# Performance work log

Measured on AMD Instinct MI355X. Metric: run time of the kernel, lower is better.

Reference implementation:

```python
import jax, jax.numpy as jnp
import numpy as np

B, L, D = 8, 2048, 1024
NH, M = 32, 16            # TTTConfig defaults: num_attention_heads=32, mini_batch_size=16
HD = D // NH              # 32
NM = L // M               # 128 mini-batches
DI = 2048                 # FFN hidden (configs.d_lower)
BASE_LR = 1.0
EPS = 1e-6


def setup_inputs() -> dict:
    key = jax.random.key(0)
    ks = jax.random.split(key, 12)
    n = lambda k, s, sc=0.02: jax.random.normal(k, s, jnp.float32) * sc
    return dict(
        enc_input=jax.random.normal(ks[0], (B, L, D), jnp.float32),
        ln0_g=jnp.ones((D,), jnp.float32), ln0_b=jnp.zeros((D,), jnp.float32),
        Wq=n(ks[1], (D, D)), Wk=n(ks[2], (D, D)), Wv=n(ks[3], (D, D)), Wo=n(ks[4], (D, D)),
        W1=n(ks[5], (NH, HD, HD)), b1=jnp.zeros((NH, 1, HD), jnp.float32),
        token_idx_delta=jnp.zeros((M,), jnp.float32),
        lr_w=n(ks[6], (NH, D)), lr_b=jnp.zeros((NH,), jnp.float32),
        ttt_ln_g=jnp.ones((NH, HD), jnp.float32), ttt_ln_b=jnp.zeros((NH, HD), jnp.float32),
        post_g=jnp.ones((D,), jnp.float32), post_b=jnp.zeros((D,), jnp.float32),
        ffn_g=jnp.ones((D,), jnp.float32), ffn_b=jnp.zeros((D,), jnp.float32),
        fw1=n(ks[7], (D, DI)), fb1=jnp.zeros((DI,), jnp.float32),
        fw2=n(ks[8], (DI, D)), fb2=jnp.zeros((D,), jnp.float32),
    )


def _layernorm(x, g, b):
    mu = x.mean(-1, keepdims=True)
    v = ((x - mu) ** 2).mean(-1, keepdims=True)
    return (x - mu) * jax.lax.rsqrt(v + EPS) * g + b


def _rope(x):
    # x: [B,NH,L,HD]; standard rotary embedding, theta=10000
    half = HD // 2
    inv = 1.0 / (10000.0 ** (jnp.arange(0, HD, 2, dtype=jnp.float32) / HD))
    pos = jnp.arange(L, dtype=jnp.float32)
    fr = pos[:, None] * inv[None, :]                    # [L, HD/2]
    emb = jnp.concatenate([fr, fr], -1)                 # [L, HD]
    cos, sin = jnp.cos(emb), jnp.sin(emb)
    rot = jnp.concatenate([-x[..., half:], x[..., :half]], -1)
    return x * cos + rot * sin


def reference(enc_input, ln0_g, ln0_b, Wq, Wk, Wv, Wo, W1, b1, token_idx_delta,
              lr_w, lr_b, ttt_ln_g, ttt_ln_b, post_g, post_b,
              ffn_g, ffn_b, fw1, fb1, fw2, fb2):
    residual = enc_input
    x = _layernorm(enc_input, ln0_g, ln0_b)

    def heads(t):  # [B,L,D] -> [B,NH,L,HD]
        return t.reshape(B, L, NH, HD).transpose(0, 2, 1, 3)

    XQ = _rope(heads(x @ Wq))
    XK = _rope(heads(x @ Wk))
    XV = heads(x @ Wv)

    # per-token learnable learning rates (sigmoid gate), token_idx schedule
    X_mb = x.reshape(B, NM, M, D)
    ttt_lr = jax.nn.sigmoid(jnp.einsum('bnkc,hc->bhnk', X_mb, lr_w) + lr_b[None, :, None, None])
    ttt_lr_eta = BASE_LR * ttt_lr / HD                               # [B,NH,NM,M]
    token_idx = jnp.clip(1.0 / jnp.arange(1, M + 1, dtype=jnp.float32) + token_idx_delta, 0.0, None)
    eta = token_idx[None, None, None, :, None] * ttt_lr_eta[:, :, :, None, :]  # [B,NH,NM,M,M]

    def to_scan(t):  # [B,NH,L,HD] -> [NM,B,NH,M,HD]
        return t.reshape(B, NH, NM, M, HD).transpose(2, 0, 1, 3, 4)

    xs = (to_scan(XQ), to_scan(XK), to_scan(XV), eta.transpose(2, 0, 1, 3, 4))

    lw = ttt_ln_g[:, None, :]   # [NH,1,HD]
    lb = ttt_ln_b[:, None, :]
    tril = jnp.tril(jnp.ones((M, M), jnp.float32))

    def ln_fwd(z):
        mu = z.mean(-1, keepdims=True)
        v = ((z - mu) ** 2).mean(-1, keepdims=True)
        return (z - mu) * jax.lax.rsqrt(v + EPS) * lw + lb

    def ln_l2_bwd(z, tgt):
        # gradient of 0.5*||LN(z)-tgt||^2 w.r.t. z (fused LN l2 backward)
        mu = z.mean(-1, keepdims=True)
        v = ((z - mu) ** 2).mean(-1, keepdims=True)
        std = jnp.sqrt(v + EPS)
        xhat = (z - mu) / std
        gxh = (xhat * lw + lb - tgt) * lw
        return (HD * gxh - gxh.sum(-1, keepdims=True)
                - xhat * (gxh * xhat).sum(-1, keepdims=True)) / (HD * std)

    W1_0 = jnp.broadcast_to(W1[None], (B, NH, HD, HD))
    b1_0 = jnp.broadcast_to(b1[None], (B, NH, 1, HD))

    def step(carry, inp):
        W, bvec = carry
        q, k, v_, e = inp                                    # [B,NH,M,HD], e: [B,NH,M,M]
        Z1 = k @ W + bvec
        grad = ln_l2_bwd(Z1, v_ - k)                         # [B,NH,M,HD]
        Attn1 = tril * (q @ k.transpose(0, 1, 3, 2))         # causal dual-form attention
        b_bar = bvec - (tril * e) @ grad
        Z1_bar = q @ W - (e * Attn1) @ grad + b_bar
        last_e = e[:, :, -1, :, None]                        # [B,NH,M,1]
        W_new = W - (last_e * k).transpose(0, 1, 3, 2) @ grad
        b_new = bvec - (last_e * grad).sum(-2, keepdims=True)
        return (W_new, b_new), q + ln_fwd(Z1_bar)

    _, outs = jax.lax.scan(step, (W1_0, b1_0), xs)           # [NM,B,NH,M,HD]
    out = outs.transpose(1, 0, 3, 2, 4).reshape(B, L, D)     # -> [B,L,D]
    out = _layernorm(out, post_g, post_b) @ Wo               # post_norm + o_proj
    out = out + residual                                     # dropout = identity (eval)

    # PositionWiseFeedForward (pre-LN, residual)
    r2 = out
    h = _layernorm(out, ffn_g, ffn_b)
    h = jax.nn.relu(h @ fw1 + fb1) @ fw2 + fb2
    return h + r2
```

## Files before the change

### kernel.cpp

```cpp
#include <hip/hip_runtime.h>
#include <hip/hip_bf16.h>
#include <stdint.h>

#define B_   8
#define L_   2048
#define D_   1024
#define NH_  32
#define M_   16
#define NM_  128
#define HD_  32
#define DI_  2048
#define BL_  16384
#define EPS_ 1e-6f

typedef __attribute__((ext_vector_type(8))) short  s16x8;
typedef __attribute__((ext_vector_type(4))) short  s16x4;
typedef __attribute__((ext_vector_type(8))) __bf16 bf16x8;
typedef __attribute__((ext_vector_type(4))) float  f32x4;
typedef __attribute__((ext_vector_type(4))) unsigned u32x4;

__device__ __forceinline__ float bf2f(short s){
  unsigned u = ((unsigned)(unsigned short)s) << 16;
  return __builtin_bit_cast(float, u);
}
__device__ __forceinline__ short f2bf(float f){
  unsigned u = __builtin_bit_cast(unsigned, f);
  u = u + 0x7FFFu + ((u >> 16) & 1u);
  return (short)(u >> 16);
}
__device__ __forceinline__ unsigned cvtpk(float lo, float hi){
  unsigned r;
  asm("v_cvt_pk_bf16_f32 %0, %1, %2" : "=v"(r) : "v"(lo), "v"(hi));
  return r;
}
template<int N>
__device__ __forceinline__ float ror_add(float v){
  const int y = __builtin_amdgcn_update_dpp(
      0, __builtin_bit_cast(int, v), 0x120 + N, 0xF, 0xF, true);
  return v + __builtin_bit_cast(float, y);
}
__device__ __forceinline__ float rsum16d(float v){
  v = ror_add<1>(v); v = ror_add<2>(v); v = ror_add<4>(v); v = ror_add<8>(v);
  return v;
}
__device__ __forceinline__ void wgbar(){
  asm volatile("s_waitcnt lgkmcnt(0)" ::: "memory");
  __builtin_amdgcn_s_barrier();
  __builtin_amdgcn_sched_barrier(0);
}
__device__ __forceinline__ void gl16(const void* g, void* l){
  __builtin_amdgcn_global_load_lds(
      (const __attribute__((address_space(1))) void*)g,
      (__attribute__((address_space(3))) void*)l, 16, 0, 0);
}

__global__ __launch_bounds__(256) void transpose_cast(
    const float* __restrict__ in, short* __restrict__ out, int R, int Cc)
{
  __shared__ float t[32][33];
  const int lx = threadIdx.x & 31, ly = threadIdx.x >> 5;
  const int r0 = blockIdx.y * 32, c0 = blockIdx.x * 32;
  #pragma unroll
  for (int s = 0; s < 4; ++s){
    const int r = ly + s*8;
    t[r][lx] = in[(size_t)(r0 + r)*Cc + c0 + lx];
  }
  __syncthreads();
  #pragma unroll
  for (int s = 0; s < 4; ++s){
    const int r = ly + s*8;
    out[(size_t)(c0 + r)*R + r0 + lx] = f2bf(t[lx][r]);
  }
}

struct TC4 { const float *s0,*s1,*s2,*s3; short *d0,*d1,*d2,*d3; };
__global__ __launch_bounds__(256) void transpose_cast4(TC4 p)
{
  __shared__ float t[32][33];
  const int z = blockIdx.z;
  const float* in = (z==0)?p.s0:(z==1)?p.s1:(z==2)?p.s2:p.s3;
  short* out      = (z==0)?p.d0:(z==1)?p.d1:(z==2)?p.d2:p.d3;
  const int lx = threadIdx.x & 31, ly = threadIdx.x >> 5;
  const int r0 = blockIdx.y * 32, c0 = blockIdx.x * 32;
  #pragma unroll
  for (int s = 0; s < 4; ++s){
    const int r = ly + s*8;
    t[r][lx] = in[(size_t)(r0 + r)*1024 + c0 + lx];
  }
  __syncthreads();
  #pragma unroll
  for (int s = 0; s < 4; ++s){
    const int r = ly + s*8;
    out[(size_t)(c0 + r)*1024 + r0 + lx] = f2bf(t[lx][r]);
  }
}

__global__ __launch_bounds__(256) void misc_prep(
    const float* __restrict__ lr_w, short* __restrict__ lrwb,
    float* __restrict__ ct, float* __restrict__ st)
{
  const int idx = blockIdx.x*256 + threadIdx.x;
  if (idx < NH_*D_){
    lrwb[idx] = f2bf(lr_w[idx]);
  } else {
    const int k = idx - NH_*D_;
    const int l = k >> 4, j = k & 15;
    const float inv = powf(10000.f, -(float)j * (1.f/16.f));
    const float fr  = (float)l * inv;
    ct[k] = cosf(fr);
    st[k] = sinf(fr);
  }
}

__global__ __launch_bounds__(256) void ln_rows(
    const float* __restrict__ in, const float* __restrict__ g,
    const float* __restrict__ bta, short* __restrict__ out)
{
  const int row = blockIdx.x, tid = threadIdx.x;
  const float4 v = ((const float4*)(in + (size_t)row*D_))[tid];
  float s  = v.x + v.y + v.z + v.w;
  float s2 = v.x*v.x + v.y*v.y + v.z*v.z + v.w*v.w;
  #pragma unroll
  for (int m = 1; m < 64; m <<= 1){ s += __shfl_xor(s, m); s2 += __shfl_xor(s2, m); }
  __shared__ float rs[4], rq[4];
  if ((tid & 63) == 0){ rs[tid>>6] = s; rq[tid>>6] = s2; }
  __syncthreads();
  s  = rs[0] + rs[1] + rs[2] + rs[3];
  s2 = rq[0] + rq[1] + rq[2] + rq[3];
  const float mu   = s  * (1.f/D_);
  const float var  = s2 * (1.f/D_) - mu*mu;
  const float rstd = rsqrtf(var + EPS_);
  const float4 gg = ((const float4*)g)[tid];
  const float4 bb = ((const float4*)bta)[tid];
  s16x4 o;
  o[0] = f2bf((v.x - mu)*rstd*gg.x + bb.x);
  o[1] = f2bf((v.y - mu)*rstd*gg.y + bb.y);
  o[2] = f2bf((v.z - mu)*rstd*gg.z + bb.z);
  o[3] = f2bf((v.w - mu)*rstd*gg.w + bb.w);
  ((s16x4*)(out + (size_t)row*D_))[tid] = o;
}

__global__ __launch_bounds__(256) void ln_rows_bf(
    const short* __restrict__ in, const float* __restrict__ g,
    const float* __restrict__ bta, short* __restrict__ out)
{
  const int row = blockIdx.x, tid = threadIdx.x;
  const s16x4 v4 = ((const s16x4*)(in + (size_t)row*D_))[tid];
  float v[4];
  #pragma unroll
  for (int e = 0; e < 4; ++e) v[e] = bf2f(v4[e]);
  float s  = v[0]+v[1]+v[2]+v[3];
  float s2 = v[0]*v[0]+v[1]*v[1]+v[2]*v[2]+v[3]*v[3];
  #pragma unroll
  for (int m = 1; m < 64; m <<= 1){ s += __shfl_xor(s, m); s2 += __shfl_xor(s2, m); }
  __shared__ float rs[4], rq[4];
  if ((tid & 63) == 0){ rs[tid>>6] = s; rq[tid>>6] = s2; }
  __syncthreads();
  s  = rs[0] + rs[1] + rs[2] + rs[3];
  s2 = rq[0] + rq[1] + rq[2] + rq[3];
  const float mu   = s  * (1.f/D_);
  const float var  = s2 * (1.f/D_) - mu*mu;
  const float rstd = rsqrtf(var + EPS_);
  const float4 gg = ((const float4*)g)[tid];
  const float4 bb = ((const float4*)bta)[tid];
  s16x4 o;
  #pragma unroll
  for (int e = 0; e < 4; ++e){
    const float gv = (e==0)?gg.x:(e==1)?gg.y:(e==2)?gg.z:gg.w;
    const float bv = (e==0)?bb.x:(e==1)?bb.y:(e==2)?bb.z:bb.w;
    o[e] = f2bf((v[e] - mu)*rstd*gv + bv);
  }
  ((s16x4*)(out + (size_t)row*D_))[tid] = o;
}

template<int ACT, int OUTBF, int BIAS, int RES, int RESB, int QKVOUT>
__global__ __launch_bounds__(512, 2) void gemm256(
    const short* __restrict__ A, const short* __restrict__ Bt,
    const float* __restrict__ bias, const float* __restrict__ res,
    const short* __restrict__ resb,
    float* __restrict__ Cf, short* __restrict__ Cb,
    const float* __restrict__ ct, const float* __restrict__ st,
    int Mr, int N, int K)
{
  __shared__ __align__(16) short As[4][8192];
  __shared__ __align__(16) short Bs[4][8192];
  const int tid  = threadIdx.x;
  const int lane = tid & 63, wid = tid >> 6;
  const int wr = wid >> 2, wc = wid & 3;
  const int nwg = gridDim.x * gridDim.y;
  const int wg  = blockIdx.y * gridDim.x + blockIdx.x;
  const int swz = (wg & 7) * (nwg >> 3) + (wg >> 3);
  const int bx  = swz % gridDim.x, by = swz / gridDim.x;
  const int row0 = by * 256, col0 = bx * 256;

  f32x4 acc[8][4] = {};

  const int kswz = (((tid & 3) ^ ((tid >> 3) & 3)) << 3);
  const short* gAb = A  + (size_t)(row0 + (tid >> 2)) * K + kswz;
  const short* gBb = Bt + (size_t)(col0 + (tid >> 2)) * K + kswz;
  short* lAb = &As[0][0] + tid*8;
  short* lBb = &Bs[0][0] + tid*8;

  auto stage = [&](int bt2, int t2){
    const size_t kb = (size_t)t2 * 32;
    gl16(gAb + kb,                   lAb + bt2*8192);
    gl16(gAb + kb + 128*(size_t)K,   lAb + bt2*8192 + 4096);
    gl16(gBb + kb,                   lBb + bt2*8192);
    gl16(gBb + kb + 128*(size_t)K,   lBb + bt2*8192 + 4096);
  };

  const int fr = lane & 15;
  const int k0 = (((lane >> 4) ^ ((lane >> 1) & 3)) << 3);

  const int nK = K >> 5;
  stage(0, 0); stage(1, 1); stage(2, 2);
  asm volatile("s_waitcnt vmcnt(8)" ::: "memory");
  __builtin_amdgcn_s_barrier();

  for (int kt = 0; kt < nK; ++kt){
    const int bt = kt & 3;
    const short* Ab = &As[0][0] + bt*8192 + wr*4096;
    const short* Bb = &Bs[0][0] + bt*8192 + (wc >> 1)*4096 + (wc & 1)*2048;
    bf16x8 af[8], bfv[4];
    #pragma unroll
    for (int m = 0; m < 8; ++m)
      af[m] = *(const bf16x8*)(Ab + (m*16 + fr)*32 + k0);
    #pragma unroll
    for (int n = 0; n < 4; ++n)
      bfv[n] = *(const bf16x8*)(Bb + (n*16 + fr)*32 + k0);
    if (kt + 3 < nK) stage((kt + 3) & 3, kt + 3);
    __builtin_amdgcn_s_setprio(1);
    #pragma unroll
    for (int m = 0; m < 8; ++m)
      #pragma unroll
      for (int n = 0; n < 4; ++n)
        acc[m][n] = __builtin_amdgcn_mfma_f32_16x16x32_bf16(af[m], bfv[n], acc[m][n], 0,0,0);
    __builtin_amdgcn_s_setprio(0);
    if (kt + 3 < nK)      asm volatile("s_waitcnt vmcnt(8)" ::: "memory");
    else if (kt + 2 < nK) asm volatile("s_waitcnt vmcnt(4)" ::: "memory");
    else if (kt + 1 < nK) asm volatile("s_waitcnt vmcnt(0)" ::: "memory");
    __builtin_amdgcn_s_barrier();
  }

  const int cr = (lane >> 4) * 4, cc = lane & 15;
  if (QKVOUT){
    const int part = col0 >> 10;
    #pragma unroll
    for (int m = 0; m < 8; ++m){
      const int gr0 = row0 + wr*128 + m*16 + cr;
      const int bidx = gr0 >> 11, l0 = gr0 & (L_-1);
      const int nn = l0 >> 4;
      if (part < 2){
        #pragma unroll
        for (int np = 0; np < 2; ++np){
          const int gc = col0 + wc*64 + np*32 + cc;
          const int hh = (gc & 1023) >> 5;
          short* tile = Cb + ((size_t)(bidx*NH_ + hh)*NM_ + nn)*2048;
          s16x4 r0v, r1v;
          #pragma unroll
          for (int r = 0; r < 4; ++r){
            const int l = l0 + r;
            const float cv = ct[l*16 + cc], sv = st[l*16 + cc];
            const float x0 = acc[m][np*2][r], x1 = acc[m][np*2+1][r];
            const short q0 = f2bf(x0*cv - x1*sv);
            const short q1 = f2bf(x1*cv + x0*sv);
            tile[part*512 + (cr + r)*32 + cc]      = q0;
            tile[part*512 + (cr + r)*32 + cc + 16] = q1;
            r0v[r] = q0; r1v[r] = q1;
          }
          if (part == 1){
            *(s16x4*)(tile + 1024 + cc*16 + cr)      = r0v;
            *(s16x4*)(tile + 1024 + (cc+16)*16 + cr) = r1v;
          }
        }
      } else {
        #pragma unroll
        for (int n = 0; n < 4; ++n){
          const int gc = col0 + wc*64 + n*16 + cc;
          const int hh = (gc & 1023) >> 5, dd = gc & 31;
          short* tile = Cb + ((size_t)(bidx*NH_ + hh)*NM_ + nn)*2048;
          s16x4 p;
          #pragma unroll
          for (int r = 0; r < 4; ++r) p[r] = f2bf(acc[m][n][r]);
          *(s16x4*)(tile + 1536 + dd*16 + cr) = p;
        }
      }
    }
    return;
  }
  #pragma unroll
  for (int m = 0; m < 8; ++m){
    #pragma unroll
    for (int n = 0; n < 4; ++n){
      const int gc = col0 + wc*64 + n*16 + cc;
      float bv = 0.f;
      if (BIAS) bv = bias[gc];
      #pragma unroll
      for (int r = 0; r < 4; ++r){
        const int gr = row0 + wr*128 + m*16 + cr + r;
        float v = acc[m][n][r] + bv;
        if (RES)  v += res[(size_t)gr*N + gc];
        if (RESB) v += bf2f(resb[(size_t)gr*N + gc]);
        if (ACT == 1) v = fmaxf(v, 0.f);
        if (OUTBF) Cb[(size_t)gr*N + gc] = f2bf(v);
        else       Cf[(size_t)gr*N + gc] = v;
      }
    }
  }
}

__global__ __launch_bounds__(256) void eta_kernel(
    const short* __restrict__ xb, const short* __restrict__ lrwb,
    const float* __restrict__ lr_b, float* __restrict__ eta)
{
  __shared__ __align__(16) short wl[NH_*1032];
  const int tid = threadIdx.x;
  const int lane = tid & 63, wv = tid >> 6;
  const int li = lane & 15, lh = lane >> 4;
  #pragma unroll
  for (int s = 0; s < 16; ++s){
    const int e = tid + 256*s;
    const int hrow = e >> 7, c = (e & 127) * 8;
    *(s16x8*)(wl + hrow*1032 + c) = ((const s16x8*)lrwb)[e];
  }
  __syncthreads();

  const int t0 = (blockIdx.x*4 + wv) * 16;
  const short* xrow = xb + (size_t)(t0 + li)*1024 + 8*lh;
  const short* w0p = wl + li*1032 + 8*lh;
  const short* w1p = wl + (16 + li)*1032 + 8*lh;
  f32x4 acc0 = {}, acc1 = {};
  #pragma unroll 4
  for (int s = 0; s < 32; ++s){
    const bf16x8 a  = *(const bf16x8*)(xrow + s*32);
    const bf16x8 b0 = *(const bf16x8*)(w0p + s*32);
    const bf16x8 b1 = *(const bf16x8*)(w1p + s*32);
    acc0 = __builtin_amdgcn_mfma_f32_16x16x32_bf16(a, b0, acc0, 0,0,0);
    acc1 = __builtin_amdgcn_mfma_f32_16x16x32_bf16(a, b1, acc1, 0,0,0);
  }
  const int t = t0 + 4*lh;
  const int bidx = t >> 11, l = t & (L_-1), n = l >> 4, im = l & 15;
  float* e0 = eta + ((size_t)(bidx*NH_ + li)*NM_ + n)*M_ + im;
  float* e1 = eta + ((size_t)(bidx*NH_ + 16 + li)*NM_ + n)*M_ + im;
  const float lb0 = lr_b[li], lb1 = lr_b[16 + li];
  #pragma unroll
  for (int r = 0; r < 4; ++r){
    e0[r] = 1.f/(1.f + __expf(-(acc0[r] + lb0))) * (1.f/32.f);
    e1[r] = 1.f/(1.f + __expf(-(acc1[r] + lb1))) * (1.f/32.f);
  }
}

__global__ __launch_bounds__(128) void scan_kernel(
    const short* __restrict__ Q5, const float* __restrict__ eta,
    const float* __restrict__ W1, const float* __restrict__ b1,
    const float* __restrict__ tdelta, const float* __restrict__ lng,
    const float* __restrict__ lnb, short* __restrict__ out)
{
  const int bh = blockIdx.x;
  const int h = bh & 31, b = bh >> 5;
  const int lane = threadIdx.x & 63;
  const int wv = threadIdx.x >> 6;
  const int li = lane & 15, lh = lane >> 4;

  __shared__ __align__(16) short WTl[2][32*40];
  __shared__ __align__(16) short GTl[2][32*24];
  __shared__ float BBl[2][2][16];
  __shared__ __align__(16) float AT[16*20];
  __shared__ __align__(16) short QLl[2][16*40];

  const short* chain = Q5 + (size_t)bh * (NM_*2048);
  const float* ech   = eta + (size_t)bh * (NM_*16);

  float lw[2], lbv[2];
  #pragma unroll
  for (int hh = 0; hh < 2; ++hh){
    lw[hh]  = lng[h*32 + 16*hh + li];
    lbv[hh] = lnb[h*32 + 16*hh + li];
  }

  if (wv == 0){
    f32x4 Wq[2][2];
    #pragma unroll
    for (int rb = 0; rb < 2; ++rb)
      #pragma unroll
      for (int cb = 0; cb < 2; ++cb)
        #pragma unroll
        for (int r = 0; r < 4; ++r)
          Wq[rb][cb][r] = W1[h*1024 + (16*rb + 4*lh + r)*32 + 16*cb + li];
    float bb[2];
    bb[0] = b1[h*32 + li];  bb[1] = b1[h*32 + 16 + li];
    const float lef = fmaxf(1.f/16.f + tdelta[15], 0.f);

    auto writeWT = [&](int sl){
      #pragma unroll
      for (int cb = 0; cb < 2; ++cb)
        #pragma unroll
        for (int rb = 0; rb < 2; ++rb){
          const unsigned p0 = cvtpk(Wq[rb][cb][0], Wq[rb][cb][1]);
          const unsigned p1 = cvtpk(Wq[rb][cb][2], Wq[rb][cb][3]);
          *(uint64_t*)(&WTl[sl][0] + (16*cb + li)*40 + 16*rb + 4*lh) =
              ((uint64_t)p1 << 32) | p0;
        }
    };
    auto readWf = [&](int sl, bf16x8* Wf){
      Wf[0] = *(const bf16x8*)(&WTl[sl][0] + li*40 + 8*lh);
      Wf[1] = *(const bf16x8*)(&WTl[sl][0] + (16 + li)*40 + 8*lh);
    };

    writeWT(0);
    if (lh == 0){ BBl[0][0][li] = bb[0]; BBl[0][1][li] = bb[1]; }
    bf16x8 Wf[2];
    readWf(0, Wf);

    struct P0 { s16x8 kA, kTq0, kTq1; s16x4 kTe0, kTe1, vTe0, vTe1;
                f32x4 lr0, lr1, lr2, lr3; };
    auto ld0 = [&](int n) -> P0 {
      const short* t = chain + (size_t)n*2048;
      const float* e = ech + n*16;
      P0 p;
      p.kA   = *(const s16x8*)(t + 512 + li*32 + 8*lh);
      p.kTq0 = *(const s16x8*)(t + 1024 + li*16 + 8*(lh & 1));
      p.kTq1 = *(const s16x8*)(t + 1024 + (16 + li)*16 + 8*(lh & 1));
      p.kTe0 = *(const s16x4*)(t + 1024 + li*16 + 4*lh);
      p.kTe1 = *(const s16x4*)(t + 1024 + (16 + li)*16 + 4*lh);
      p.vTe0 = *(const s16x4*)(t + 1536 + li*16 + 4*lh);
      p.vTe1 = *(const s16x4*)(t + 1536 + (16 + li)*16 + 4*lh);
      p.lr0 = *(const f32x4*)(e);     p.lr1 = *(const f32x4*)(e + 4);
      p.lr2 = *(const f32x4*)(e + 8); p.lr3 = *(const f32x4*)(e + 12);
      return p;
    };

    P0 cur = ld0(0);
    wgbar();

    const int gcol = (8*lh) & 15;
    #pragma unroll 1
    for (int n = 0; n < NM_; ++n){
      const int sl = n & 1;
      P0 nxt = ld0(n + 1 < NM_ ? n + 1 : NM_ - 1);
      const bf16x8 kAf = __builtin_bit_cast(bf16x8, cur.kA);

      f32x4 zac[2];
      #pragma unroll
      for (int hh = 0; hh < 2; ++hh){
        f32x4 c0; c0[0]=bb[hh]; c0[1]=bb[hh]; c0[2]=bb[hh]; c0[3]=bb[hh];
        zac[hh] = __builtin_amdgcn_mfma_f32_16x16x32_bf16(kAf, Wf[hh], c0, 0,0,0);
      }

      float xh[2][4], grad[2][4], rstdv[4];
      #pragma unroll
      for (int r = 0; r < 4; ++r){
        float s  = rsum16d(zac[0][r] + zac[1][r]);
        float q2 = rsum16d(zac[0][r]*zac[0][r] + zac[1][r]*zac[1][r]);
        const float mu  = s * (1.f/32.f);
        const float var = q2 * (1.f/32.f) - mu*mu;
        const float rstd = rsqrtf(var + EPS_);
        rstdv[r] = rstd;
        xh[0][r] = (zac[0][r] - mu) * rstd;
        xh[1][r] = (zac[1][r] - mu) * rstd;
      }
      #pragma unroll
      for (int r = 0; r < 4; ++r){
        const float t0 = bf2f(cur.vTe0[r]) - bf2f(cur.kTe0[r]);
        const float t1 = bf2f(cur.vTe1[r]) - bf2f(cur.kTe1[r]);
        const float g0 = (xh[0][r]*lw[0] + lbv[0] - t0)*lw[0];
        const float g1 = (xh[1][r]*lw[1] + lbv[1] - t1)*lw[1];
        const float sg  = rsum16d(g0 + g1);
        const float sgx = rsum16d(g0*xh[0][r] + g1*xh[1][r]);
        const float f = rstdv[r] * (1.f/32.f);
        grad[0][r] = (32.f*g0 - sg - xh[0][r]*sgx) * f;
        grad[1][r] = (32.f*g1 - sg - xh[1][r]*sgx) * f;
      }

      #pragma unroll
      for (int hh = 0; hh < 2; ++hh){
        const unsigned p0 = cvtpk(grad[hh][0], grad[hh][1]);
        const unsigned p1 = cvtpk(grad[hh][2], grad[hh][3]);
        *(uint64_t*)(&GTl[sl][0] + (16*hh + li)*24 + 4*lh) =
            ((uint64_t)p1 << 32) | p0;
      }
      bf16x8 gf[2];
      gf[0] = *(const bf16x8*)(&GTl[sl][0] + li*24 + gcol);
      gf[1] = *(const bf16x8*)(&GTl[sl][0] + (16 + li)*24 + gcol);

      const f32x4 plA = (lh & 1) ? cur.lr2 : cur.lr0;
      const f32x4 plB = (lh & 1) ? cur.lr3 : cur.lr1;
      #pragma unroll
      for (int rb = 0; rb < 2; ++rb){
        const s16x8 kq = rb ? cur.kTq1 : cur.kTq0;
        float av8[8];
        #pragma unroll
        for (int jj = 0; jj < 8; ++jj){
          const float lrv = (jj < 4) ? plA[jj] : plB[jj - 4];
          av8[jj] = (lh < 2) ? -lef * lrv * bf2f(kq[jj]) : 0.f;
        }
        u32x4 auv;
        auv[0] = cvtpk(av8[0], av8[1]); auv[1] = cvtpk(av8[2], av8[3]);
        auv[2] = cvtpk(av8[4], av8[5]); auv[3] = cvtpk(av8[6], av8[7]);
        const bf16x8 af = __builtin_bit_cast(bf16x8, auv);
        #pragma unroll
        for (int cb = 0; cb < 2; ++cb)
          Wq[rb][cb] = __builtin_amdgcn_mfma_f32_16x16x32_bf16(af, gf[cb], Wq[rb][cb], 0,0,0);
      }

      writeWT(sl ^ 1);
      readWf(sl ^ 1, Wf);

      f32x4 lrq;
      { const f32x4 t0 = (lh & 1) ? cur.lr1 : cur.lr0;
        const f32x4 t1 = (lh & 1) ? cur.lr3 : cur.lr2;
        lrq = (lh & 2) ? t1 : t0; }
      #pragma unroll
      for (int hh = 0; hh < 2; ++hh){
        float t = 0.f;
        #pragma unroll
        for (int r = 0; r < 4; ++r) t += lrq[r]*grad[hh][r];
        t += __shfl_xor(t, 16); t += __shfl_xor(t, 32);
        bb[hh] -= lef * t;
      }
      if (lh == 0){ BBl[sl ^ 1][0][li] = bb[0]; BBl[sl ^ 1][1][li] = bb[1]; }
      cur = nxt;
      wgbar();
    }
  } else {
    const float tok_i = fmaxf(1.f/(float)(li+1) + tdelta[li], 0.f);
    short* outp = out + (size_t)b*L_*D_ + h*32;
    const int gcol = (8*lh) & 15;

    struct P1 { s16x8 qA, kA; f32x4 lr0, lr1, lr2, lr3; };
    auto ld1 = [&](int n) -> P1 {
      const short* t = chain + (size_t)n*2048;
      const float* e = ech + n*16;
      P1 p;
      p.qA = *(const s16x8*)(t + li*32 + 8*lh);
      p.kA = *(const s16x8*)(t + 512 + li*32 + 8*lh);
      p.lr0 = *(const f32x4*)(e);     p.lr1 = *(const f32x4*)(e + 4);
      p.lr2 = *(const f32x4*)(e + 8); p.lr3 = *(const f32x4*)(e + 12);
      return p;
    };

    auto outln = [&](int n, const f32x4* yac){
      #pragma unroll
      for (int r = 0; r < 4; ++r){
        const float s  = rsum16d(yac[0][r] + yac[1][r]);
        const float q2 = rsum16d(yac[0][r]*yac[0][r] + yac[1][r]*yac[1][r]);
        const float mu   = s * (1.f/32.f);
        const float var  = q2 * (1.f/32.f) - mu*mu;
        const float rstd = rsqrtf(var + EPS_);
        const int row = 4*lh + r;
        #pragma unroll
        for (int hh = 0; hh < 2; ++hh){
          const float qv = bf2f(QLl[n & 1][row*40 + 16*hh + li]);
          const float o  = qv + (yac[hh][r] - mu)*rstd*lw[hh] + lbv[hh];
          outp[(size_t)(n*16 + row)*D_ + 16*hh + li] = f2bf(o);
        }
      }
    };

    P1 cur = ld1(0);
    wgbar();

    f32x4 yprev[2] = {};
    bf16x8 pPrev = {};
    #pragma unroll 1
    for (int n = 0; n < NM_; ++n){
      const int sl = n & 1;
      bf16x8 Wf0 = *(const bf16x8*)(&WTl[sl][0] + li*40 + 8*lh);
      bf16x8 Wf1 = *(const bf16x8*)(&WTl[sl][0] + (16 + li)*40 + 8*lh);
      const float bb0 = BBl[sl][0][li];
      const float bb1 = BBl[sl][1][li];

      if (n > 0){
        bf16x8 gf0 = *(const bf16x8*)(&GTl[sl ^ 1][0] + li*24 + gcol);
        bf16x8 gf1 = *(const bf16x8*)(&GTl[sl ^ 1][0] + (16 + li)*24 + gcol);
        yprev[0] = __builtin_amdgcn_mfma_f32_16x16x32_bf16(pPrev, gf0, yprev[0], 0,0,0);
        yprev[1] = __builtin_amdgcn_mfma_f32_16x16x32_bf16(pPrev, gf1, yprev[1], 0,0,0);
        outln(n - 1, yprev);
      }

      P1 nxt = ld1(n + 1 < NM_ ? n + 1 : NM_ - 1);
      const bf16x8 qAf = __builtin_bit_cast(bf16x8, cur.qA);
      const bf16x8 kAf = __builtin_bit_cast(bf16x8, cur.kA);

      *(s16x8*)(&QLl[sl][0] + li*40 + 8*lh) = cur.qA;

      f32x4 aac = {};
      aac = __builtin_amdgcn_mfma_f32_16x16x32_bf16(qAf, kAf, aac, 0,0,0);
      #pragma unroll
      for (int r = 0; r < 4; ++r)
        AT[(4*lh + r)*20 + li] = aac[r];

      f32x4 arA = {}, arB = {};
      if (lh < 2){
        arA = *(const f32x4*)(AT + li*20 + 8*lh);
        arB = *(const f32x4*)(AT + li*20 + 8*lh + 4);
      }
      const f32x4 plA = (lh & 1) ? cur.lr2 : cur.lr0;
      const f32x4 plB = (lh & 1) ? cur.lr3 : cur.lr1;
      float pv[8];
      #pragma unroll
      for (int jj = 0; jj < 8; ++jj){
        const float av  = (jj < 4) ? arA[jj] : arB[jj - 4];
        const float lrv = (jj < 4) ? plA[jj] : plB[jj - 4];
        const bool ok = (lh < 2) && (8*lh + jj <= li);
        pv[jj] = ok ? -tok_i * lrv * (1.f + av) : 0.f;
      }
      u32x4 ppv;
      ppv[0] = cvtpk(pv[0], pv[1]); ppv[1] = cvtpk(pv[2], pv[3]);
      ppv[2] = cvtpk(pv[4], pv[5]); ppv[3] = cvtpk(pv[6], pv[7]);
      pPrev = __builtin_bit_cast(bf16x8, ppv);

      { f32x4 c0; c0[0]=bb0; c0[1]=bb0; c0[2]=bb0; c0[3]=bb0;
        yprev[0] = __builtin_amdgcn_mfma_f32_16x16x32_bf16(qAf, Wf0, c0, 0,0,0); }
      { f32x4 c0; c0[0]=bb1; c0[1]=bb1; c0[2]=bb1; c0[3]=bb1;
        yprev[1] = __builtin_amdgcn_mfma_f32_16x16x32_bf16(qAf, Wf1, c0, 0,0,0); }

      cur = nxt;
      wgbar();
    }
    {
      const int sl = (NM_ - 1) & 1;
      bf16x8 gf0 = *(const bf16x8*)(&GTl[sl][0] + li*24 + gcol);
      bf16x8 gf1 = *(const bf16x8*)(&GTl[sl][0] + (16 + li)*24 + gcol);
      yprev[0] = __builtin_amdgcn_mfma_f32_16x16x32_bf16(pPrev, gf0, yprev[0], 0,0,0);
      yprev[1] = __builtin_amdgcn_mfma_f32_16x16x32_bf16(pPrev, gf1, yprev[1], 0,0,0);
      outln(NM_ - 1, yprev);
    }
  }
}

extern "C" void kernel_launch(void* const* d_in, const int* in_sizes, int n_in,
                              void* d_out, int out_size, void* d_ws, size_t ws_size,
                              hipStream_t stream)
{
  const float* enc    = (const float*)d_in[0];
  const float* ln0_g  = (const float*)d_in[1];
  const float* ln0_b  = (const float*)d_in[2];
  const float* Wq     = (const float*)d_in[3];
  const float* Wk     = (const float*)d_in[4];
  const float* Wv     = (const float*)d_in[5];
  const float* Wo     = (const float*)d_in[6];
  const float* W1     = (const float*)d_in[7];
  const float* b1     = (const float*)d_in[8];
  const float* tdelta = (const float*)d_in[9];
  const float* lr_w   = (const float*)d_in[10];
  const float* lr_b   = (const float*)d_in[11];
  const float* ttt_g  = (const float*)d_in[12];
  const float* ttt_b  = (const float*)d_in[13];
  const float* post_g = (const float*)d_in[14];
  const float* post_b = (const float*)d_in[15];
  const float* ffn_g  = (const float*)d_in[16];
  const float* ffn_b  = (const float*)d_in[17];
  const float* fw1    = (const float*)d_in[18];
  const float* fb1    = (const float*)d_in[19];
  const float* fw2    = (const float*)d_in[20];
  const float* fb2    = (const float*)d_in[21];

  char* ws = (char*)d_ws;
  short* Q5    = (short*)(ws + 0);
  short* XB    = (short*)(ws + 134217728);
  short* SCANB = (short*)(ws + 134217728);
  short* WQKVT = (short*)(ws + 167772160);
  short* WOT   = (short*)(ws + 174063616);
  short* FW1T  = (short*)(ws + 176160768);
  short* FW2T  = (short*)(ws + 180355072);
  short* LRWB  = (short*)(ws + 184549376);
  float* CT    = (float*)(ws + 184614912);
  float* ST    = (float*)(ws + 184745984);
  float* ETA   = (float*)(ws + 184877056);
  short* YB    = (short*)(ws + 0);
  short* HB    = (short*)(ws + 33554432);
  short* T1    = (short*)(ws + 67108864);
  short* R2B   = (short*)(ws + 134217728);
  float* R2    = (float*)d_out;

  dim3 b256(256), b512(512);
  TC4 tc;
  tc.s0 = Wq; tc.s1 = Wk; tc.s2 = Wv; tc.s3 = Wo;
  tc.d0 = WQKVT; tc.d1 = WQKVT + 1048576; tc.d2 = WQKVT + 2097152; tc.d3 = WOT;
  transpose_cast4<<<dim3(32,32,4), b256, 0, stream>>>(tc);
  transpose_cast<<<dim3(64,32), b256, 0, stream>>>(fw1, FW1T, D_, DI_);
  transpose_cast<<<dim3(32,64), b256, 0, stream>>>(fw2, FW2T, DI_, D_);
  misc_prep<<<dim3(256), b256, 0, stream>>>(lr_w, LRWB, CT, ST);

  ln_rows<<<BL_, b256, 0, stream>>>(enc, ln0_g, ln0_b, XB);
  gemm256<0,0,0,0,0,1><<<dim3(12,64), b512, 0, stream>>>(XB, WQKVT, nullptr, nullptr, nullptr,
                                                         nullptr, Q5, CT, ST, BL_, 3072, D_);
  eta_kernel<<<dim3(256), b256, 0, stream>>>(XB, LRWB, lr_b, ETA);
  scan_kernel<<<dim3(256), dim3(128), 0, stream>>>(Q5, ETA, W1, b1, tdelta,
                                                   ttt_g, ttt_b, SCANB);
  ln_rows_bf<<<BL_, b256, 0, stream>>>(SCANB, post_g, post_b, YB);
  gemm256<0,1,0,1,0,0><<<dim3(4,64), b512, 0, stream>>>(YB, WOT, nullptr, enc, nullptr,
                                                        nullptr, R2B, nullptr, nullptr, BL_, D_, D_);
  ln_rows_bf<<<BL_, b256, 0, stream>>>(R2B, ffn_g, ffn_b, HB);
  gemm256<1,1,1,0,0,0><<<dim3(8,64), b512, 0, stream>>>(HB, FW1T, fb1, nullptr, nullptr,
                                                        nullptr, T1, nullptr, nullptr, BL_, DI_, D_);
  gemm256<0,0,1,0,1,0><<<dim3(4,64), b512, 0, stream>>>(T1, FW2T, fb2, nullptr, R2B,
                                                        R2, nullptr, nullptr, nullptr, BL_, D_, DI_);
}
```

Before: 510.1 us.

## Split scan output work across two consumer wavefronts alternating mini-batches

The scan kernel grows from two to three wavefronts per block. The first wavefront still runs the sequential weight-update chain, and the output-side work is now split between two consumer waves that take even and odd mini-batches. This aims to stop the consumer work from lengthening each step of the serial chain. The loop is restructured to run NM+1 phases with a block barrier each phase, and the double-buffered LDS slots must now stay valid across the producer's lead.

```diff
diff --git a/kernel.cpp b/kernel.cpp
--- a/kernel.cpp
+++ b/kernel.cpp
@@ -350,7 +350,7 @@
   }
 }
 
-__global__ __launch_bounds__(128) void scan_kernel(
+__global__ __launch_bounds__(192) void scan_kernel(
     const short* __restrict__ Q5, const float* __restrict__ eta,
     const float* __restrict__ W1, const float* __restrict__ b1,
     const float* __restrict__ tdelta, const float* __restrict__ lng,
@@ -435,94 +435,98 @@
 
     const int gcol = (8*lh) & 15;
     #pragma unroll 1
-    for (int n = 0; n < NM_; ++n){
-      const int sl = n & 1;
-      P0 nxt = ld0(n + 1 < NM_ ? n + 1 : NM_ - 1);
-      const bf16x8 kAf = __builtin_bit_cast(bf16x8, cur.kA);
-
-      f32x4 zac[2];
-      #pragma unroll
-      for (int hh = 0; hh < 2; ++hh){
-        f32x4 c0; c0[0]=bb[hh]; c0[1]=bb[hh]; c0[2]=bb[hh]; c0[3]=bb[hh];
-        zac[hh] = __builtin_amdgcn_mfma_f32_16x16x32_bf16(kAf, Wf[hh], c0, 0,0,0);
+    for (int p = 0; p <= NM_; ++p){
+      if (p < NM_){
+        const int n = p;
+        const int sl = n & 1;
+        P0 nxt = ld0(n + 1 < NM_ ? n + 1 : NM_ - 1);
+        const bf16x8 kAf = __builtin_bit_cast(bf16x8, cur.kA);
+
+        f32x4 zac[2];
+        #pragma unroll
+        for (int hh = 0; hh < 2; ++hh){
+          f32x4 c0; c0[0]=bb[hh]; c0[1]=bb[hh]; c0[2]=bb[hh]; c0[3]=bb[hh];
+          zac[hh] = __builtin_amdgcn_mfma_f32_16x16x32_bf16(kAf, Wf[hh], c0, 0,0,0);
+        }
+
+        float xh[2][4], grad[2][4], rstdv[4];
+        #pragma unroll
+        for (int r = 0; r < 4; ++r){
+          float s  = rsum16d(zac[0][r] + zac[1][r]);
+          float q2 = rsum16d(zac[0][r]*zac[0][r] + zac[1][r]*zac[1][r]);
+          const float mu  = s * (1.f/32.f);
+          const float var = q2 * (1.f/32.f) - mu*mu;
+          const float rstd = rsqrtf(var + EPS_);
+          rstdv[r] = rstd;
+          xh[0][r] = (zac[0][r] - mu) * rstd;
+          xh[1][r] = (zac[1][r] - mu) * rstd;
+        }
+        #pragma unroll
+        for (int r = 0; r < 4; ++r){
+          const float t0 = bf2f(cur.vTe0[r]) - bf2f(cur.kTe0[r]);
+          const float t1 = bf2f(cur.vTe1[r]) - bf2f(cur.kTe1[r]);
+          const float g0 = (xh[0][r]*lw[0] + lbv[0] - t0)*lw[0];
+          const float g1 = (xh[1][r]*lw[1] + lbv[1] - t1)*lw[1];
+          const float sg  = rsum16d(g0 + g1);
+          const float sgx = rsum16d(g0*xh[0][r] + g1*xh[1][r]);
+          const float f = rstdv[r] * (1.f/32.f);
+          grad[0][r] = (32.f*g0 - sg - xh[0][r]*sgx) * f;
+          grad[1][r] = (32.f*g1 - sg - xh[1][r]*sgx) * f;
+        }
+
+        #pragma unroll
+        for (int hh = 0; hh < 2; ++hh){
+          const unsigned p0 = cvtpk(grad[hh][0], grad[hh][1]);
+          const unsigned p1 = cvtpk(grad[hh][2], grad[hh][3]);
+          *(uint64_t*)(&GTl[sl][0] + (16*hh + li)*24 + 4*lh) =
+              ((uint64_t)p1 << 32) | p0;
+        }
+        bf16x8 gf[2];
+        gf[0] = *(const bf16x8*)(&GTl[sl][0] + li*24 + gcol);
+        gf[1] = *(const bf16x8*)(&GTl[sl][0] + (16 + li)*24 + gcol);
+
+        const f32x4 plA = (lh & 1) ? cur.lr2 : cur.lr0;
+        const f32x4 plB = (lh & 1) ? cur.lr3 : cur.lr1;
+        #pragma unroll
+        for (int rb = 0; rb < 2; ++rb){
+          const s16x8 kq = rb ? cur.kTq1 : cur.kTq0;
+          float av8[8];
+          #pragma unroll
+          for (int jj = 0; jj < 8; ++jj){
+            const float lrv = (jj < 4) ? plA[jj] : plB[jj - 4];
+            av8[jj] = (lh < 2) ? -lef * lrv * bf2f(kq[jj]) : 0.f;
+          }
+          u32x4 auv;
+          auv[0] = cvtpk(av8[0], av8[1]); auv[1] = cvtpk(av8[2], av8[3]);
+          auv[2] = cvtpk(av8[4], av8[5]); auv[3] = cvtpk(av8[6], av8[7]);
+          const bf16x8 af = __builtin_bit_cast(bf16x8, auv);
+          #pragma unroll
+          for (int cb = 0; cb < 2; ++cb)
+            Wq[rb][cb] = __builtin_amdgcn_mfma_f32_16x16x32_bf16(af, gf[cb], Wq[rb][cb], 0,0,0);
+        }
+
+        writeWT(sl ^ 1);
+        readWf(sl ^ 1, Wf);
+
+        f32x4 lrq;
+        { const f32x4 t0 = (lh & 1) ? cur.lr1 : cur.lr0;
+          const f32x4 t1 = (lh & 1) ? cur.lr3 : cur.lr2;
+          lrq = (lh & 2) ? t1 : t0; }
+        #pragma unroll
+        for (int hh = 0; hh < 2; ++hh){
+          float t = 0.f;
+          #pragma unroll
+          for (int r = 0; r < 4; ++r) t += lrq[r]*grad[hh][r];
+          t += __shfl_xor(t, 16); t += __shfl_xor(t, 32);
+          bb[hh] -= lef * t;
+        }
+        if (lh == 0){ BBl[sl ^ 1][0][li] = bb[0]; BBl[sl ^ 1][1][li] = bb[1]; }
+        cur = nxt;
       }
-
-      float xh[2][4], grad[2][4], rstdv[4];
-      #pragma unroll
-      for (int r = 0; r < 4; ++r){
-        float s  = rsum16d(zac[0][r] + zac[1][r]);
-        float q2 = rsum16d(zac[0][r]*zac[0][r] + zac[1][r]*zac[1][r]);
-        const float mu  = s * (1.f/32.f);
-        const float var = q2 * (1.f/32.f) - mu*mu;
-        const float rstd = rsqrtf(var + EPS_);
-        rstdv[r] = rstd;
-        xh[0][r] = (zac[0][r] - mu) * rstd;
-        xh[1][r] = (zac[1][r] - mu) * rstd;
-      }
-      #pragma unroll
-      for (int r = 0; r < 4; ++r){
-        const float t0 = bf2f(cur.vTe0[r]) - bf2f(cur.kTe0[r]);
-        const float t1 = bf2f(cur.vTe1[r]) - bf2f(cur.kTe1[r]);
-        const float g0 = (xh[0][r]*lw[0] + lbv[0] - t0)*lw[0];
-        const float g1 = (xh[1][r]*lw[1] + lbv[1] - t1)*lw[1];
-        const float sg  = rsum16d(g0 + g1);
-        const float sgx = rsum16d(g0*xh[0][r] + g1*xh[1][r]);
-        const float f = rstdv[r] * (1.f/32.f);
-        grad[0][r] = (32.f*g0 - sg - xh[0][r]*sgx) * f;
-        grad[1][r] = (32.f*g1 - sg - xh[1][r]*sgx) * f;
-      }
-
-      #pragma unroll
-      for (int hh = 0; hh < 2; ++hh){
-        const unsigned p0 = cvtpk(grad[hh][0], grad[hh][1]);
-        const unsigned p1 = cvtpk(grad[hh][2], grad[hh][3]);
-        *(uint64_t*)(&GTl[sl][0] + (16*hh + li)*24 + 4*lh) =
-            ((uint64_t)p1 << 32) | p0;
-      }
-      bf16x8 gf[2];
-      gf[0] = *(const bf16x8*)(&GTl[sl][0] + li*24 + gcol);
-      gf[1] = *(const bf16x8*)(&GTl[sl][0] + (16 + li)*24 + gcol);
-
-      const f32x4 plA = (lh & 1) ? cur.lr2 : cur.lr0;
-      const f32x4 plB = (lh & 1) ? cur.lr3 : cur.lr1;
-      #pragma unroll
-      for (int rb = 0; rb < 2; ++rb){
-        const s16x8 kq = rb ? cur.kTq1 : cur.kTq0;
-        float av8[8];
-        #pragma unroll
-        for (int jj = 0; jj < 8; ++jj){
-          const float lrv = (jj < 4) ? plA[jj] : plB[jj - 4];
-          av8[jj] = (lh < 2) ? -lef * lrv * bf2f(kq[jj]) : 0.f;
-        }
-        u32x4 auv;
-        auv[0] = cvtpk(av8[0], av8[1]); auv[1] = cvtpk(av8[2], av8[3]);
-        auv[2] = cvtpk(av8[4], av8[5]); auv[3] = cvtpk(av8[6], av8[7]);
-        const bf16x8 af = __builtin_bit_cast(bf16x8, auv);
-        #pragma unroll
-        for (int cb = 0; cb < 2; ++cb)
-          Wq[rb][cb] = __builtin_amdgcn_mfma_f32_16x16x32_bf16(af, gf[cb], Wq[rb][cb], 0,0,0);
-      }
-
-      writeWT(sl ^ 1);
-      readWf(sl ^ 1, Wf);
-
-      f32x4 lrq;
-      { const f32x4 t0 = (lh & 1) ? cur.lr1 : cur.lr0;
-        const f32x4 t1 = (lh & 1) ? cur.lr3 : cur.lr2;
-        lrq = (lh & 2) ? t1 : t0; }
-      #pragma unroll
-      for (int hh = 0; hh < 2; ++hh){
-        float t = 0.f;
-        #pragma unroll
-        for (int r = 0; r < 4; ++r) t += lrq[r]*grad[hh][r];
-        t += __shfl_xor(t, 16); t += __shfl_xor(t, 32);
-        bb[hh] -= lef * t;
-      }
-      if (lh == 0){ BBl[sl ^ 1][0][li] = bb[0]; BBl[sl ^ 1][1][li] = bb[1]; }
-      cur = nxt;
       wgbar();
     }
   } else {
+    const int par = wv - 1;
     const float tok_i = fmaxf(1.f/(float)(li+1) + tdelta[li], 0.f);
     short* outp = out + (size_t)b*L_*D_ + h*32;
     const int gcol = (8*lh) & 15;
@@ -557,74 +561,69 @@
       }
     };
 
-    P1 cur = ld1(0);
+    P1 cur = ld1(par);
     wgbar();
 
-    f32x4 yprev[2] = {};
-    bf16x8 pPrev = {};
+    f32x4 ycur[2] = {};
+    bf16x8 pCur = {};
     #pragma unroll 1
-    for (int n = 0; n < NM_; ++n){
-      const int sl = n & 1;
-      bf16x8 Wf0 = *(const bf16x8*)(&WTl[sl][0] + li*40 + 8*lh);
-      bf16x8 Wf1 = *(const bf16x8*)(&WTl[sl][0] + (16 + li)*40 + 8*lh);
-      const float bb0 = BBl[sl][0][li];
-      const float bb1 = BBl[sl][1][li];
-
-      if (n > 0){
-        bf16x8 gf0 = *(const bf16x8*)(&GTl[sl ^ 1][0] + li*24 + gcol);
-        bf16x8 gf1 = *(const bf16x8*)(&GTl[sl ^ 1][0] + (16 + li)*24 + gcol);
-        yprev[0] = __builtin_amdgcn_mfma_f32_16x16x32_bf16(pPrev, gf0, yprev[0], 0,0,0);
-        yprev[1] = __builtin_amdgcn_mfma_f32_16x16x32_bf16(pPrev, gf1, yprev[1], 0,0,0);
-        outln(n - 1, yprev);
+    for (int p = 0; p <= NM_; ++p){
+      if (p >= 1 && ((p - 1) & 1) == par){
+        const int m = p - 1;
+        const int sl = m & 1;
+        bf16x8 gf0 = *(const bf16x8*)(&GTl[sl][0] + li*24 + gcol);
+        bf16x8 gf1 = *(const bf16x8*)(&GTl[sl][0] + (16 + li)*24 + gcol);
+        ycur[0] = __builtin_amdgcn_mfma_f32_16x16x32_bf16(pCur, gf0, ycur[0], 0,0,0);
+        ycur[1] = __builtin_amdgcn_mfma_f32_16x16x32_bf16(pCur, gf1, ycur[1], 0,0,0);
+        outln(m, ycur);
       }
-
-      P1 nxt = ld1(n + 1 < NM_ ? n + 1 : NM_ - 1);
-      const bf16x8 qAf = __builtin_bit_cast(bf16x8, cur.qA);
-      const bf16x8 kAf = __builtin_bit_cast(bf16x8, cur.kA);
-
-      *(s16x8*)(&QLl[sl][0] + li*40 + 8*lh) = cur.qA;
-
-      f32x4 aac = {};
-      aac = __builtin_amdgcn_mfma_f32_16x16x32_bf16(qAf, kAf, aac, 0,0,0);
-      #pragma unroll
-      for (int r = 0; r < 4; ++r)
-        AT[(4*lh + r)*20 + li] = aac[r];
-
-      f32x4 arA = {}, arB = {};
-      if (lh < 2){
-        arA = *(const f32x4*)(AT + li*20 + 8*lh);
-        arB = *(const f32x4*)(AT + li*20 + 8*lh + 4);
+      if (p < NM_ && (p & 1) == par){
+        const int sl = p & 1;
+        bf16x8 Wf0 = *(const bf16x8*)(&WTl[sl][0] + li*40 + 8*lh);
+        bf16x8 Wf1 = *(const bf16x8*)(&WTl[sl][0] + (16 + li)*40 + 8*lh);
+        const float bb0 = BBl[sl][0][li];
+        const float bb1 = BBl[sl][1][li];
+
+        P1 nxt = ld1(p + 2 < NM_ ? p + 2 : p);
+        const bf16x8 qAf = __builtin_bit_cast(bf16x8, cur.qA);
+        const bf16x8 kAf = __builtin_bit_cast(bf16x8, cur.kA);
+
+        *(s16x8*)(&QLl[sl][0] + li*40 + 8*lh) = cur.qA;
+
+        f32x4 aac = {};
+        aac = __builtin_amdgcn_mfma_f32_16x16x32_bf16(qAf, kAf, aac, 0,0,0);
+        #pragma unroll
+        for (int r = 0; r < 4; ++r)
+          AT[(4*lh + r)*20 + li] = aac[r];
+
+        f32x4 arA = {}, arB = {};
+        if (lh < 2){
+          arA = *(const f32x4*)(AT + li*20 + 8*lh);
+          arB = *(const f32x4*)(AT + li*20 + 8*lh + 4);
+        }
+        const f32x4 plA = (lh & 1) ? cur.lr2 : cur.lr0;
+        const f32x4 plB = (lh & 1) ? cur.lr3 : cur.lr1;
+        float pv[8];
+        #pragma unroll
+        for (int jj = 0; jj < 8; ++jj){
+          const float av  = (jj < 4) ? arA[jj] : arB[jj - 4];
+          const float lrv = (jj < 4) ? plA[jj] : plB[jj - 4];
+          const bool ok = (lh < 2) && (8*lh + jj <= li);
+          pv[jj] = ok ? -tok_i * lrv * (1.f + av) : 0.f;
+        }
+        u32x4 ppv;
+        ppv[0] = cvtpk(pv[0], pv[1]); ppv[1] = cvtpk(pv[2], pv[3]);
+        ppv[2] = cvtpk(pv[4], pv[5]); ppv[3] = cvtpk(pv[6], pv[7]);
+        pCur = __builtin_bit_cast(bf16x8, ppv);
+
+        { f32x4 c0; c0[0]=bb0; c0[1]=bb0; c0[2]=bb0; c0[3]=bb0;
+          ycur[0] = __builtin_amdgcn_mfma_f32_16x16x32_bf16(qAf, Wf0, c0, 0,0,0); }
+        { f32x4 c0; c0[0]=bb1; c0[1]=bb1; c0[2]=bb1; c0[3]=bb1;
+          ycur[1] = __builtin_amdgcn_mfma_f32_16x16x32_bf16(qAf, Wf1, c0, 0,0,0); }
+
+        cur = nxt;
       }
-      const f32x4 plA = (lh & 1) ? cur.lr2 : cur.lr0;
-      const f32x4 plB = (lh & 1) ? cur.lr3 : cur.lr1;
-      float pv[8];
-      #pragma unroll
-      for (int jj = 0; jj < 8; ++jj){
-        const float av  = (jj < 4) ? arA[jj] : arB[jj - 4];
-        const float lrv = (jj < 4) ? plA[jj] : plB[jj - 4];
-        const bool ok = (lh < 2) && (8*lh + jj <= li);
-        pv[jj] = ok ? -tok_i * lrv * (1.f + av) : 0.f;
-      }
-      u32x4 ppv;
-      ppv[0] = cvtpk(pv[0], pv[1]); ppv[1] = cvtpk(pv[2], pv[3]);
-      ppv[2] = cvtpk(pv[4], pv[5]); ppv[3] = cvtpk(pv[6], pv[7]);
-      pPrev = __builtin_bit_cast(bf16x8, ppv);
-
-      { f32x4 c0; c0[0]=bb0; c0[1]=bb0; c0[2]=bb0; c0[3]=bb0;
-        yprev[0] = __builtin_amdgcn_mfma_f32_16x16x32_bf16(qAf, Wf0, c0, 0,0,0); }
-      { f32x4 c0; c0[0]=bb1; c0[1]=bb1; c0[2]=bb1; c0[3]=bb1;
-        yprev[1] = __builtin_amdgcn_mfma_f32_16x16x32_bf16(qAf, Wf1, c0, 0,0,0); }
-
-      cur = nxt;
       wgbar();
-    }
-    {
-      const int sl = (NM_ - 1) & 1;
-      bf16x8 gf0 = *(const bf16x8*)(&GTl[sl][0] + li*24 + gcol);
-      bf16x8 gf1 = *(const bf16x8*)(&GTl[sl][0] + (16 + li)*24 + gcol);
-      yprev[0] = __builtin_amdgcn_mfma_f32_16x16x32_bf16(pPrev, gf0, yprev[0], 0,0,0);
-      yprev[1] = __builtin_amdgcn_mfma_f32_16x16x32_bf16(pPrev, gf1, yprev[1], 0,0,0);
-      outln(NM_ - 1, yprev);
     }
   }
 }
@@ -687,7 +686,7 @@
   gemm256<0,0,0,0,0,1><<<dim3(12,64), b512, 0, stream>>>(XB, WQKVT, nullptr, nullptr, nullptr,
                                                          nullptr, Q5, CT, ST, BL_, 3072, D_);
   eta_kernel<<<dim3(256), b256, 0, stream>>>(XB, LRWB, lr_b, ETA);
-  scan_kernel<<<dim3(256), dim3(128), 0, stream>>>(Q5, ETA, W1, b1, tdelta,
+  scan_kernel<<<dim3(256), dim3(192), 0, stream>>>(Q5, ETA, W1, b1, tdelta,
                                                    ttt_g, ttt_b, SCANB);
   ln_rows_bf<<<BL_, b256, 0, stream>>>(SCANB, post_g, post_b, YB);
   gemm256<0,1,0,1,0,0><<<dim3(4,64), b512, 0, stream>>>(YB, WOT, nullptr, enc, nullptr,
```

New measurement: 504.8 us. Within noise of the previous version (-1.0%).
